# Kernel tuning notes

Measured on AMD Instinct MI355X. Metric: run time of the kernel, lower is better.

Reference implementation:

```python
import jax, jax.numpy as jnp
import numpy as np

B, S, D = 4, 2048, 1024
NUM_CODES = 16384


def setup_inputs() -> dict:
    key = jax.random.key(0)
    k1, k2 = jax.random.split(key)
    inputs = jax.random.normal(k1, (B, S, D), dtype=jnp.float32)
    codebook = jax.random.normal(k2, (NUM_CODES, D), dtype=jnp.float32)
    return {"inputs": inputs, "codebook": codebook, "kcodes": 8}


def reference(inputs, codebook, kcodes):
    # logits = -cdist(inputs, codebook, p=2); squared distance is monotonic
    # with euclidean distance, so top-k indices are identical (no sqrt needed).
    x2 = jnp.sum(inputs * inputs, axis=-1, keepdims=True)        # [B,S,1]
    c2 = jnp.sum(codebook * codebook, axis=-1)                   # [C]
    xc = jnp.einsum('bsd,cd->bsc', inputs, codebook)             # [B,S,C]
    logits = -(x2 - 2.0 * xc + c2)                               # -squared dist
    _, codebook_ids = jax.lax.top_k(logits, kcodes)              # [B,S,K]
    gathered = codebook[codebook_ids]                            # [B,S,K,D]
    outputs = gathered.sum(axis=-2) / kcodes                     # [B,S,D]
    return outputs, codebook_ids
```

## Files before the change

kernel.cpp:

```cpp
#include <hip/hip_runtime.h>
#include <hip/hip_bf16.h>
#include <float.h>

#define R_TOTAL 8192
#define D_DIM   1024
#define C_TOTAL 16384
#define KSEL    8
#define XN  ((size_t)R_TOTAL * D_DIM)
#define CBN ((size_t)C_TOTAL * D_DIM)
#define NSPLIT  8
#define SEGC    (C_TOTAL / NSPLIT)
#define NCHUNK  (SEGC / 256)
#define NKT     (NCHUNK * 16)
#define NC_RES  24

typedef __attribute__((ext_vector_type(8)))  short short8v;
typedef __attribute__((ext_vector_type(16))) float f32x16;
typedef __attribute__((ext_vector_type(8)))  unsigned short ushort8;

__device__ __forceinline__ unsigned short f2bf(float f) {
  unsigned u = __float_as_uint(f);
  u = (u + 0x7fffu + ((u >> 16) & 1u)) >> 16;
  return (unsigned short)u;
}

__device__ __forceinline__ void gload_lds16(const void* g, void* l) {
  __builtin_amdgcn_global_load_lds((const __attribute__((address_space(1))) void*)g,
                                   (__attribute__((address_space(3))) void*)l, 16, 0, 0);
}

__global__ void cvt_kernel(const float* __restrict__ X, const float* __restrict__ CB,
                           unsigned short* __restrict__ Xb, unsigned short* __restrict__ CBb) {
  size_t e = ((size_t)blockIdx.x * 256 + threadIdx.x) * 8;
  const float* src; unsigned short* dst; size_t off;
  if (e < XN) { src = X;  dst = Xb;  off = e; }
  else        { src = CB; dst = CBb; off = e - XN; }
  float4 v0 = *(const float4*)(src + off);
  float4 v1 = *(const float4*)(src + off + 4);
  ushort8 o;
  o[0]=f2bf(v0.x); o[1]=f2bf(v0.y); o[2]=f2bf(v0.z); o[3]=f2bf(v0.w);
  o[4]=f2bf(v1.x); o[5]=f2bf(v1.y); o[6]=f2bf(v1.z); o[7]=f2bf(v1.w);
  *(ushort8*)(dst + off) = o;
}

__global__ void c2_kernel(const float* __restrict__ cb, float* __restrict__ c2) {
  const int wave = threadIdx.x >> 6;
  const int lane = threadIdx.x & 63;
  const int code = blockIdx.x * 4 + wave;
  const float* row = cb + (size_t)code * D_DIM;
  float s = 0.f;
  #pragma unroll
  for (int i = 0; i < D_DIM / 64; ++i) { float v = row[lane + i * 64]; s += v * v; }
  #pragma unroll
  for (int off = 32; off >= 1; off >>= 1) s += __shfl_xor(s, off, 64);
  if (lane == 0) c2[code] = s;
}

__global__ __launch_bounds__(512, 2)
void gemm_topk_kernel(const unsigned short* __restrict__ Xb,
                      const unsigned short* __restrict__ CBb,
                      const float* __restrict__ c2g,
                      float* __restrict__ pval, int* __restrict__ pid) {
  extern __shared__ char smem[];
  float* c2s = (float*)(smem + 131072);

  const int t   = threadIdx.x;
  const int wid = t >> 6, l = t & 63;
  const int wr  = wid >> 2;
  const int wc  = wid & 3;
  const int l31 = l & 31, hi = l >> 5;

  const int xt    = blockIdx.x & 31;
  const int seg   = blockIdx.x >> 5;
  const int xbase = xt * 256;
  const int cb0   = seg * SEGC;

  *(float4*)&c2s[t * 4] = *(const float4*)(c2g + cb0 + t * 4);

  const int srow = t >> 3;
  const int sswz = (((t & 7) * 16) ^ ((srow & 7) << 4)) >> 1;
  const int fswz = (l & 7) << 4;

  f32x16 acc[4][2];
  float tv[2][KSEL]; int ti[2][KSEL];
  #pragma unroll
  for (int fm = 0; fm < 4; ++fm)
    #pragma unroll
    for (int fn = 0; fn < 2; ++fn)
      #pragma unroll
      for (int r = 0; r < 16; ++r) acc[fm][fn][r] = 0.f;
  #pragma unroll
  for (int fn = 0; fn < 2; ++fn)
    #pragma unroll
    for (int q = 0; q < KSEL; ++q) { tv[fn][q] = -FLT_MAX; ti[fn][q] = 0; }

  auto STAGE_A = [&](int g) {
    const int kbase = (g & 15) * 64;
    const int arow0 = cb0 + (g >> 4) * 256;
    char* As = smem + (g & 1) * 32768;
    #pragma unroll
    for (int i = 0; i < 4; ++i)
      gload_lds16(CBb + (size_t)(arow0 + i * 64 + srow) * D_DIM + kbase + sswz,
                  As + (i * 512 + t) * 16);
  };
  auto STAGE_X = [&](int g) {
    const int kbase = (g & 15) * 64;
    char* Xs = smem + 65536 + (g & 1) * 32768;
    #pragma unroll
    for (int i = 0; i < 4; ++i)
      gload_lds16(Xb + (size_t)(xbase + i * 64 + srow) * D_DIM + kbase + sswz,
                  Xs + (i * 512 + t) * 16);
  };

  STAGE_A(0); STAGE_X(0);
  asm volatile("s_waitcnt vmcnt(0) lgkmcnt(0)" ::: "memory");
  __builtin_amdgcn_s_barrier();

  for (int g = 0; g < NKT; ++g) {
    const char* As = smem + (g & 1) * 32768;
    const char* Xs = smem + 65536 + (g & 1) * 32768;

    #pragma unroll
    for (int p = 0; p < 4; ++p) {
      short8v av[4], bv[2];
      const int kb = (p * 32 + hi * 16) ^ fswz;
      #pragma unroll
      for (int fm = 0; fm < 4; ++fm)
        av[fm] = *(const short8v*)(As + (wr * 128 + fm * 32 + l31) * 128 + kb);
      #pragma unroll
      for (int fn = 0; fn < 2; ++fn)
        bv[fn] = *(const short8v*)(Xs + (wc * 64 + fn * 32 + l31) * 128 + kb);

      if (p == 0 && g + 1 < NKT) STAGE_A(g + 1);
      if (p == 1 && g + 1 < NKT) STAGE_X(g + 1);

      __builtin_amdgcn_s_barrier();

      __builtin_amdgcn_s_setprio(1);
      #pragma unroll
      for (int fm = 0; fm < 4; ++fm)
        #pragma unroll
        for (int fn = 0; fn < 2; ++fn)
          acc[fm][fn] = __builtin_amdgcn_mfma_f32_32x32x16_bf16(
              av[fm], bv[fn], acc[fm][fn], 0, 0, 0);
      __builtin_amdgcn_s_setprio(0);

      if (p == 3)
        asm volatile("s_waitcnt vmcnt(0)" ::: "memory");
      __builtin_amdgcn_s_barrier();
    }

    if ((g & 15) == 15) {
      const int ch = g >> 4;
      #pragma unroll
      for (int fm = 0; fm < 4; ++fm) {
        const int rloc = ch * 256 + wr * 128 + fm * 32 + hi * 4;
        const int idb  = cb0 + ch * 256 + wr * 128 + fm * 32 + hi * 4;
        #pragma unroll
        for (int q = 0; q < 4; ++q) {
          const float4 cq = *(const float4*)&c2s[rloc + q * 8];
          #pragma unroll
          for (int fn = 0; fn < 2; ++fn) {
            #pragma unroll
            for (int r = 0; r < 4; ++r) {
              const float c2v = (r == 0) ? cq.x : (r == 1) ? cq.y : (r == 2) ? cq.z : cq.w;
              const float s = 2.f * acc[fm][fn][q * 4 + r] - c2v;
              if (s > tv[fn][KSEL - 1]) {
                float cv = s; int ci = idb + q * 8 + r;
                #pragma unroll
                for (int q2 = 0; q2 < KSEL; ++q2) {
                  if (cv > tv[fn][q2]) {
                    const float t0 = tv[fn][q2]; tv[fn][q2] = cv; cv = t0;
                    const int   t1 = ti[fn][q2]; ti[fn][q2] = ci; ci = t1;
                  }
                }
              }
            }
          }
        }
      }
      #pragma unroll
      for (int fm = 0; fm < 4; ++fm)
        #pragma unroll
        for (int fn = 0; fn < 2; ++fn)
          #pragma unroll
          for (int r = 0; r < 16; ++r) acc[fm][fn][r] = 0.f;
    }
  }

  asm volatile("s_waitcnt vmcnt(0) lgkmcnt(0)" ::: "memory");
  __builtin_amdgcn_s_barrier();
  float* mv = (float*)smem;
  int*   mi = (int*)(smem + 32768);
  #pragma unroll
  for (int fn = 0; fn < 2; ++fn) {
    const int xrL = wc * 64 + fn * 32 + l31;
    const int li  = wr * 2 + hi;
    #pragma unroll
    for (int q = 0; q < KSEL; ++q) {
      mv[xrL * 32 + li * 8 + q] = tv[fn][q];
      mi[xrL * 32 + li * 8 + q] = ti[fn][q];
    }
  }
  __syncthreads();
  if (t < 256) {
    float bvv[KSEL]; int bii[KSEL];
    #pragma unroll
    for (int q = 0; q < KSEL; ++q) { bvv[q] = -FLT_MAX; bii[q] = 0x7fffffff; }
    for (int c = 0; c < 32; ++c) {
      float cv = mv[t * 32 + c]; int ci = mi[t * 32 + c];
      if (cv > bvv[KSEL - 1] || (cv == bvv[KSEL - 1] && ci < bii[KSEL - 1])) {
        #pragma unroll
        for (int q = 0; q < KSEL; ++q) {
          if (cv > bvv[q] || (cv == bvv[q] && ci < bii[q])) {
            const float t0 = bvv[q]; bvv[q] = cv; cv = t0;
            const int   t1 = bii[q]; bii[q] = ci; ci = t1;
          }
        }
      }
    }
    const size_t base = ((size_t)(xbase + t) * NSPLIT + seg) * KSEL;
    #pragma unroll
    for (int q = 0; q < KSEL; ++q) { pval[base + q] = bvv[q]; pid[base + q] = bii[q]; }
  }
}

__global__ __launch_bounds__(256)
void rescore_kernel(const float* __restrict__ X, const float* __restrict__ CB,
                    const float* __restrict__ c2g,
                    const float* __restrict__ pval, const int* __restrict__ pid,
                    float* __restrict__ out, float* __restrict__ out_ids, int nsplit) {
  const int row = blockIdx.x;
  const int t = threadIdx.x;
  __shared__ float xs[D_DIM];
  __shared__ int   scid[NC_RES];
  __shared__ float sv[NC_RES];
  __shared__ int   topid[KSEL];

  *(float4*)&xs[t * 4] = *(const float4*)(X + (size_t)row * D_DIM + t * 4);

  const int ncand = nsplit * KSEL;
  const int NC = NC_RES < ncand ? NC_RES : ncand;

  if (t < 64) {
    float v = -FLT_MAX; int idv = 0x7fffffff;
    if (t < ncand) {
      v   = pval[(size_t)row * ncand + t];
      idv = pid[(size_t)row * ncand + t];
    }
    for (int it = 0; it < NC; ++it) {
      float bv = v; int bid = idv;
      #pragma unroll
      for (int off = 32; off >= 1; off >>= 1) {
        float ov = __shfl_xor(bv, off, 64);
        int   oi = __shfl_xor(bid, off, 64);
        if (ov > bv || (ov == bv && oi < bid)) { bv = ov; bid = oi; }
      }
      if (t == 0) scid[it] = bid;
      if (idv == bid) v = -FLT_MAX;
    }
  }
  __syncthreads();

  const int w = t >> 6, ln = t & 63;
  for (int c = w; c < NC; c += 4) {
    const int id = scid[c];
    const float* cr = CB + (size_t)id * D_DIM;
    float s = 0.f;
    #pragma unroll
    for (int i = 0; i < 4; ++i) {
      const float4 cv = *(const float4*)(cr + ln * 4 + i * 256);
      const float4 xv = *(const float4*)&xs[ln * 4 + i * 256];
      s += cv.x * xv.x + cv.y * xv.y + cv.z * xv.z + cv.w * xv.w;
    }
    #pragma unroll
    for (int off = 32; off >= 1; off >>= 1) s += __shfl_xor(s, off, 64);
    if (ln == 0) sv[c] = 2.f * s - c2g[id];
  }
  __syncthreads();

  if (t == 0) {
    float bv[KSEL]; int bi[KSEL];
    #pragma unroll
    for (int q = 0; q < KSEL; ++q) { bv[q] = -FLT_MAX; bi[q] = 0x7fffffff; }
    for (int c = 0; c < NC; ++c) {
      float cv = sv[c]; int ci = scid[c];
      #pragma unroll
      for (int q = 0; q < KSEL; ++q) {
        if (cv > bv[q] || (cv == bv[q] && ci < bi[q])) {
          const float t0 = bv[q]; bv[q] = cv; cv = t0;
          const int   t1 = bi[q]; bi[q] = ci; ci = t1;
        }
      }
    }
    #pragma unroll
    for (int q = 0; q < KSEL; ++q) {
      topid[q] = bi[q];
      out_ids[(size_t)row * KSEL + q] = (float)bi[q];
    }
  }
  __syncthreads();

  float4 a = {0.f, 0.f, 0.f, 0.f};
  #pragma unroll
  for (int q = 0; q < KSEL; ++q) {
    const float4 cv = *(const float4*)(CB + (size_t)topid[q] * D_DIM + t * 4);
    a.x += cv.x; a.y += cv.y; a.z += cv.z; a.w += cv.w;
  }
  a.x *= 0.125f; a.y *= 0.125f; a.z *= 0.125f; a.w *= 0.125f;
  *(float4*)(out + (size_t)row * D_DIM + t * 4) = a;
}

extern "C" void kernel_launch(void* const* d_in, const int* in_sizes, int n_in,
                              void* d_out, int out_size, void* d_ws, size_t ws_size,
                              hipStream_t stream) {
  const float* X  = (const float*)d_in[0];
  const float* CB = (const float*)d_in[1];

  float* out     = (float*)d_out;
  float* out_ids = out + XN;

  const size_t XbB  = XN * 2;
  const size_t CBbB = CBN * 2;
  const size_t c2B  = C_TOTAL * 4;
  const size_t pvB  = (size_t)R_TOTAL * NSPLIT * KSEL * 4;

  char* p = (char*)d_ws;
  unsigned short* Xb;
  unsigned short* CBb;
  if (ws_size >= XbB + CBbB + c2B + 2 * pvB) {
    Xb  = (unsigned short*)p; p += XbB;
    CBb = (unsigned short*)p; p += CBbB;
  } else {
    CBb = (unsigned short*)d_out;
    Xb  = (unsigned short*)p; p += XbB;
  }
  float* c2   = (float*)p; p += c2B;
  float* pval = (float*)p; p += pvB;
  int*   pid  = (int*)p;

  hipLaunchKernelGGL(cvt_kernel, dim3((unsigned)((XN + CBN) / 8 / 256)), dim3(256), 0, stream,
                     X, CB, Xb, CBb);
  hipLaunchKernelGGL(c2_kernel, dim3(C_TOTAL / 4), dim3(256), 0, stream, CB, c2);
  hipLaunchKernelGGL(gemm_topk_kernel, dim3(32 * NSPLIT), dim3(512), 136 * 1024, stream,
                     Xb, CBb, c2, pval, pid);
  hipLaunchKernelGGL(rescore_kernel, dim3(R_TOTAL), dim3(256), 0, stream,
                     X, CB, c2, pval, pid, out, out_ids, NSPLIT);
}
```

Before: 610.6 us.

## Double-buffer LDS fragment registers to overlap reads with MFMA

Restructures the inner K loop so each sub-step reads the next set of A/X fragments from LDS into alternate registers while MFMAs run on the previously loaded set, and prefetches the next tile's first fragments before the final MFMA batch. The aim is to hide LDS read latency behind matrix math and cut barrier stalls. Sched barriers pin the intended ordering. The extra fragment registers raise register pressure, and the correctness of the cross-tile prefetch depends on barrier placement around the global-to-LDS staging.

```diff
diff --git a/kernel.cpp b/kernel.cpp
--- a/kernel.cpp
+++ b/kernel.cpp
@@ -112,43 +112,66 @@
                   Xs + (i * 512 + t) * 16);
   };
 
+  short8v avE[4], bvE[2], avO[4], bvO[2];
+
+#define READ_FRAGS(AV, BV, ABUF, XBUF, P)                                       \
+  {                                                                             \
+    const int kb_ = ((P) * 32 + hi * 16) ^ fswz;                                \
+    _Pragma("unroll")                                                           \
+    for (int fm_ = 0; fm_ < 4; ++fm_)                                           \
+      AV[fm_] = *(const short8v*)((ABUF) +                                      \
+                    (wr * 128 + fm_ * 32 + l31) * 128 + kb_);                   \
+    _Pragma("unroll")                                                           \
+    for (int fn_ = 0; fn_ < 2; ++fn_)                                           \
+      BV[fn_] = *(const short8v*)((XBUF) +                                      \
+                    (wc * 64 + fn_ * 32 + l31) * 128 + kb_);                    \
+  }
+
+#define MFMA8(AV, BV)                                                           \
+  {                                                                             \
+    __builtin_amdgcn_s_setprio(1);                                              \
+    _Pragma("unroll")                                                           \
+    for (int fm_ = 0; fm_ < 4; ++fm_)                                           \
+      _Pragma("unroll")                                                         \
+      for (int fn_ = 0; fn_ < 2; ++fn_)                                         \
+        acc[fm_][fn_] = __builtin_amdgcn_mfma_f32_32x32x16_bf16(                \
+            AV[fm_], BV[fn_], acc[fm_][fn_], 0, 0, 0);                          \
+    __builtin_amdgcn_s_setprio(0);                                              \
+    __builtin_amdgcn_sched_barrier(0);                                          \
+  }
+
   STAGE_A(0); STAGE_X(0);
   asm volatile("s_waitcnt vmcnt(0) lgkmcnt(0)" ::: "memory");
   __builtin_amdgcn_s_barrier();
+  __builtin_amdgcn_sched_barrier(0);
+  READ_FRAGS(avE, bvE, (const char*)smem, (const char*)smem + 65536, 0);
 
   for (int g = 0; g < NKT; ++g) {
-    const char* As = smem + (g & 1) * 32768;
-    const char* Xs = smem + 65536 + (g & 1) * 32768;
-
-    #pragma unroll
-    for (int p = 0; p < 4; ++p) {
-      short8v av[4], bv[2];
-      const int kb = (p * 32 + hi * 16) ^ fswz;
-      #pragma unroll
-      for (int fm = 0; fm < 4; ++fm)
-        av[fm] = *(const short8v*)(As + (wr * 128 + fm * 32 + l31) * 128 + kb);
-      #pragma unroll
-      for (int fn = 0; fn < 2; ++fn)
-        bv[fn] = *(const short8v*)(Xs + (wc * 64 + fn * 32 + l31) * 128 + kb);
-
-      if (p == 0 && g + 1 < NKT) STAGE_A(g + 1);
-      if (p == 1 && g + 1 < NKT) STAGE_X(g + 1);
-
-      __builtin_amdgcn_s_barrier();
-
-      __builtin_amdgcn_s_setprio(1);
-      #pragma unroll
-      for (int fm = 0; fm < 4; ++fm)
-        #pragma unroll
-        for (int fn = 0; fn < 2; ++fn)
-          acc[fm][fn] = __builtin_amdgcn_mfma_f32_32x32x16_bf16(
-              av[fm], bv[fn], acc[fm][fn], 0, 0, 0);
-      __builtin_amdgcn_s_setprio(0);
-
-      if (p == 3)
-        asm volatile("s_waitcnt vmcnt(0)" ::: "memory");
-      __builtin_amdgcn_s_barrier();
-    }
+    const char* As  = smem + (g & 1) * 32768;
+    const char* Xs  = smem + 65536 + (g & 1) * 32768;
+    const char* Asn = smem + ((g + 1) & 1) * 32768;
+    const char* Xsn = smem + 65536 + ((g + 1) & 1) * 32768;
+    const bool more = (g + 1 < NKT);
+
+    READ_FRAGS(avO, bvO, As, Xs, 1);
+    if (more) STAGE_A(g + 1);
+    __builtin_amdgcn_s_barrier();
+    MFMA8(avE, bvE);
+
+    READ_FRAGS(avE, bvE, As, Xs, 2);
+    if (more) STAGE_X(g + 1);
+    __builtin_amdgcn_s_barrier();
+    MFMA8(avO, bvO);
+
+    READ_FRAGS(avO, bvO, As, Xs, 3);
+    __builtin_amdgcn_s_barrier();
+    MFMA8(avE, bvE);
+
+    asm volatile("s_waitcnt vmcnt(0)" ::: "memory");
+    __builtin_amdgcn_s_barrier();
+    __builtin_amdgcn_sched_barrier(0);
+    if (more) READ_FRAGS(avE, bvE, Asn, Xsn, 0);
+    MFMA8(avO, bvO);
 
     if ((g & 15) == 15) {
       const int ch = g >> 4;
@@ -188,6 +211,9 @@
     }
   }
 
+#undef READ_FRAGS
+#undef MFMA8
+
   asm volatile("s_waitcnt vmcnt(0) lgkmcnt(0)" ::: "memory");
   __builtin_amdgcn_s_barrier();
   float* mv = (float*)smem;
```

Result: faster. 594.2 us (-2.7%).
